# Kernel optimization log

Measured on AMD Instinct MI355X. Metric: run time of the kernel, lower is better.

## Reference

```python
import jax, jax.numpy as jnp
import numpy as np

N = 100000
E = 1600000
D_IN = 128
D_OUT = 128
NEG_SLOPE = 0.01  # PyTorch LeakyReLU default


def setup_inputs() -> dict:
    key = jax.random.key(0)
    ks = jax.random.split(key, 6)
    x = jax.random.normal(ks[0], (N, D_IN), dtype=jnp.float32)
    src = jax.random.randint(ks[1], (E,), 0, N, dtype=jnp.int32)
    dst = jax.random.randint(ks[2], (E,), 0, N, dtype=jnp.int32)
    e_attn = jax.random.uniform(ks[3], (E,), dtype=jnp.float32)
    # Xavier-normal-ish init for linear weights
    std = float(np.sqrt(2.0 / (D_IN + D_OUT)))
    W1 = jax.random.normal(ks[4], (D_OUT, D_IN), dtype=jnp.float32) * std
    W2 = jax.random.normal(ks[5], (D_OUT, D_IN), dtype=jnp.float32) * std
    b1 = jnp.zeros((D_OUT,), dtype=jnp.float32)
    b2 = jnp.zeros((D_OUT,), dtype=jnp.float32)
    return {"x": x, "src": src, "dst": dst, "e_attn": e_attn,
            "W1": W1, "b1": b1, "W2": W2, "b2": b2}


def leaky_relu(v):
    return jnp.where(v >= 0, v, NEG_SLOPE * v)


def reference(x, src, dst, e_attn, W1, b1, W2, b2):
    # Edge-weighted gather-scatter: h_n[d] = sum_{e: dst(e)=d} a_e * x[src(e)]
    msgs = x[src] * e_attn[:, None]                      # [E, D_IN]
    h_n = jax.ops.segment_sum(msgs, dst, num_segments=N)  # [N, D_IN]
    # Bi-interaction: LeakyReLU(W1(x + h_n)) + LeakyReLU(W2(x * h_n))
    add_part = leaky_relu(jnp.einsum('nd,od->no', x + h_n, W1) + b1)
    mul_part = leaky_relu(jnp.einsum('nd,od->no', x * h_n, W2) + b2)
    return add_part + mul_part  # dropout p=0.0 -> identity
```

## Files before the change

### kernel.cpp

```cpp
#include <hip/hip_runtime.h>

#define N_NODES 100000
#define E_EDGES 1600000
#define D 128
#define AP 132
#define ASTR 136

typedef short s16x8 __attribute__((ext_vector_type(8)));
typedef float f32x4 __attribute__((ext_vector_type(4)));

__device__ __forceinline__ unsigned short f2bf(float f) {
    union { float f; unsigned u; } v;
    v.f = f;
    unsigned r = v.u + 0x7FFFu + ((v.u >> 16) & 1u);
    return (unsigned short)(r >> 16);
}

__device__ __forceinline__ float bf2f(unsigned short u) {
    union { unsigned u; float f; } v;
    v.u = ((unsigned)u) << 16;
    return v.f;
}

__device__ __forceinline__ float lrelu(float v) {
    return v >= 0.0f ? v : 0.01f * v;
}

__global__ __launch_bounds__(256) void xconv_kernel(
    const float* __restrict__ x, unsigned short* __restrict__ xbf) {
    int idx = blockIdx.x * 256 + threadIdx.x;
    const float4* xp = (const float4*)(x) + (size_t)idx * 2;
    float4 a = xp[0], b = xp[1];
    ushort4 lo, hi;
    lo.x = f2bf(a.x); lo.y = f2bf(a.y); lo.z = f2bf(a.z); lo.w = f2bf(a.w);
    hi.x = f2bf(b.x); hi.y = f2bf(b.y); hi.z = f2bf(b.z); hi.w = f2bf(b.w);
    ushort4* dp = (ushort4*)(xbf) + (size_t)idx * 2;
    dp[0] = lo; dp[1] = hi;
}

__global__ __launch_bounds__(256) void hist_kernel(
    const int* __restrict__ dst, int* __restrict__ cnt,
    unsigned char* __restrict__ rank, int E, int stride) {
    int e = blockIdx.x * 256 + threadIdx.x;
    if (e < E) rank[e] = (unsigned char)atomicAdd(&cnt[(size_t)dst[e] * stride], 1);
}

__global__ __launch_bounds__(256) void scanA_kernel(
    const int* __restrict__ cnt, int* __restrict__ off,
    int* __restrict__ bsum, int n, int stride) {
    __shared__ int tmp[256];
    int gid = blockIdx.x * 256 + threadIdx.x;
    int v = (gid < n) ? cnt[(size_t)gid * stride] : 0;
    tmp[threadIdx.x] = v;
    __syncthreads();
    for (int ofs = 1; ofs < 256; ofs <<= 1) {
        int t = (threadIdx.x >= ofs) ? tmp[threadIdx.x - ofs] : 0;
        __syncthreads();
        tmp[threadIdx.x] += t;
        __syncthreads();
    }
    int incl = tmp[threadIdx.x];
    if (gid < n) off[gid] = incl - v;
    if (threadIdx.x == 255) bsum[blockIdx.x] = incl;
}

__global__ __launch_bounds__(512) void scanB_kernel(int* __restrict__ bsum, int nb) {
    __shared__ int tmp[512];
    int v = (threadIdx.x < nb) ? bsum[threadIdx.x] : 0;
    tmp[threadIdx.x] = v;
    __syncthreads();
    for (int ofs = 1; ofs < 512; ofs <<= 1) {
        int t = (threadIdx.x >= ofs) ? tmp[threadIdx.x - ofs] : 0;
        __syncthreads();
        tmp[threadIdx.x] += t;
        __syncthreads();
    }
    if (threadIdx.x < nb) bsum[threadIdx.x] = tmp[threadIdx.x] - v;
}

__global__ __launch_bounds__(256) void scanC_kernel(
    const int* __restrict__ bsumExcl, int* __restrict__ off, int n, int E) {
    int gid = blockIdx.x * 256 + threadIdx.x;
    if (gid < n) off[gid] += bsumExcl[gid >> 8];
    if (gid == 0) off[n] = E;
}

__global__ __launch_bounds__(256) void fill_kernel(
    const int* __restrict__ src, const int* __restrict__ dst,
    const float* __restrict__ ea, const int* __restrict__ off,
    const unsigned char* __restrict__ rank, int2* __restrict__ csr, int E) {
    int e = blockIdx.x * 256 + threadIdx.x;
    if (e >= E) return;
    int d = dst[e];
    int pos = off[d] + (int)rank[e];
    csr[pos] = make_int2(src[e], __float_as_int(ea[e]));
}

__global__ __launch_bounds__(256, 4) void fused_gemm_kernel(
    const unsigned short* __restrict__ xbf, const int2* __restrict__ csr,
    const int* __restrict__ off, const unsigned short* __restrict__ Wswz,
    const float* __restrict__ b1, const float* __restrict__ b2,
    float* __restrict__ out) {
    __shared__ unsigned short A[2][64 * ASTR];

    const int n0 = blockIdx.x * 64;
    const int t = threadIdx.x;
    const int lane = t & 63;
    const int wv = t >> 6;
    const int half = lane >> 5;
    const int li = lane & 31;

    s16x8 Bf[2][2][4];
    float bb1[2], bb2[2];
#pragma unroll
    for (int ci = 0; ci < 2; ++ci) {
        int ct = wv + ci * 4;
        bb1[ci] = b1[ct * 16 + (lane & 15)];
        bb2[ci] = b2[ct * 16 + (lane & 15)];
#pragma unroll
        for (int mat = 0; mat < 2; ++mat)
#pragma unroll
            for (int ks = 0; ks < 4; ++ks)
                Bf[ci][mat][ks] = *(const s16x8*)(
                    Wswz + ((size_t)(((mat * 4 + ks) * 8 + ct) * 64 + lane)) * 8);
    }

    for (int j = 0; j < 16; ++j) {
        int row = wv * 16 + j;
        int node = n0 + row;
        float4 hacc = make_float4(0.f, 0.f, 0.f, 0.f);
        if (node < N_NODES) {
            int beg = off[node];
            int end = off[node + 1];
            float4 acc1 = make_float4(0.f, 0.f, 0.f, 0.f);
            int i = beg + half;
            for (; i + 2 < end; i += 4) {
                int2 p0 = csr[i];
                int2 p1 = csr[i + 2];
                float a0 = __int_as_float(p0.y);
                float a1 = __int_as_float(p1.y);
                ushort4 v0 = ((const ushort4*)(xbf + (size_t)p0.x * D))[li];
                ushort4 v1 = ((const ushort4*)(xbf + (size_t)p1.x * D))[li];
                hacc.x += a0 * bf2f(v0.x); hacc.y += a0 * bf2f(v0.y);
                hacc.z += a0 * bf2f(v0.z); hacc.w += a0 * bf2f(v0.w);
                acc1.x += a1 * bf2f(v1.x); acc1.y += a1 * bf2f(v1.y);
                acc1.z += a1 * bf2f(v1.z); acc1.w += a1 * bf2f(v1.w);
            }
            if (i < end) {
                int2 p0 = csr[i];
                float a0 = __int_as_float(p0.y);
                ushort4 v0 = ((const ushort4*)(xbf + (size_t)p0.x * D))[li];
                hacc.x += a0 * bf2f(v0.x); hacc.y += a0 * bf2f(v0.y);
                hacc.z += a0 * bf2f(v0.z); hacc.w += a0 * bf2f(v0.w);
            }
            hacc.x += acc1.x; hacc.y += acc1.y;
            hacc.z += acc1.z; hacc.w += acc1.w;
        }
        float4 oth;
        oth.x = __shfl(hacc.x, lane ^ 32);
        oth.y = __shfl(hacc.y, lane ^ 32);
        oth.z = __shfl(hacc.z, lane ^ 32);
        oth.w = __shfl(hacc.w, lane ^ 32);
        hacc.x += oth.x; hacc.y += oth.y; hacc.z += oth.z; hacc.w += oth.w;

        if (half == 0) {
            ushort4 av, mv;
            if (node < N_NODES) {
                ushort4 xu = ((const ushort4*)(xbf + (size_t)node * D))[li];
                float4 xv = make_float4(bf2f(xu.x), bf2f(xu.y), bf2f(xu.z), bf2f(xu.w));
                av.x = f2bf(xv.x + hacc.x); av.y = f2bf(xv.y + hacc.y);
                av.z = f2bf(xv.z + hacc.z); av.w = f2bf(xv.w + hacc.w);
                mv.x = f2bf(xv.x * hacc.x); mv.y = f2bf(xv.y * hacc.y);
                mv.z = f2bf(xv.z * hacc.z); mv.w = f2bf(xv.w * hacc.w);
            } else {
                av = make_ushort4(0, 0, 0, 0);
                mv = make_ushort4(0, 0, 0, 0);
            }
            *(ushort4*)&A[0][row * ASTR + li * 4] = av;
            *(ushort4*)&A[1][row * ASTR + li * 4] = mv;
        }
    }

    __syncthreads();

    const int quad = lane >> 4;
    const int kq = quad * 8;

#pragma unroll
    for (int mt = 0; mt < 4; ++mt) {
        f32x4 acc[2][2];
#pragma unroll
        for (int ci = 0; ci < 2; ++ci)
#pragma unroll
            for (int p = 0; p < 2; ++p) acc[ci][p] = (f32x4){0.f, 0.f, 0.f, 0.f};

        const int arow = mt * 16 + (lane & 15);
#pragma unroll
        for (int ks = 0; ks < 4; ++ks) {
            s16x8 a0 = *(const s16x8*)&A[0][arow * ASTR + ks * 32 + kq];
            s16x8 a1 = *(const s16x8*)&A[1][arow * ASTR + ks * 32 + kq];
#pragma unroll
            for (int ci = 0; ci < 2; ++ci) {
                acc[ci][0] = __builtin_amdgcn_mfma_f32_16x16x32_bf16(
                    a0, Bf[ci][0][ks], acc[ci][0], 0, 0, 0);
                acc[ci][1] = __builtin_amdgcn_mfma_f32_16x16x32_bf16(
                    a1, Bf[ci][1][ks], acc[ci][1], 0, 0, 0);
            }
        }

#pragma unroll
        for (int ci = 0; ci < 2; ++ci) {
            int oc = (wv + ci * 4) * 16 + (lane & 15);
#pragma unroll
            for (int r = 0; r < 4; ++r) {
                int node = n0 + mt * 16 + quad * 4 + r;
                if (node < N_NODES) {
                    float v = lrelu(acc[ci][0][r] + bb1[ci])
                            + lrelu(acc[ci][1][r] + bb2[ci]);
                    out[(size_t)node * D + oc] = v;
                }
            }
        }
    }
}

__global__ __launch_bounds__(256) void gather_f32_kernel(
    const float* __restrict__ x, const int2* __restrict__ csr,
    const int* __restrict__ off, float* __restrict__ h) {
    int node = blockIdx.x * 4 + (threadIdx.x >> 6);
    int lane = threadIdx.x & 63;
    int beg = off[node];
    int end = off[node + 1];
    float2 acc0 = make_float2(0.f, 0.f);
    float2 acc1 = make_float2(0.f, 0.f);
    int e = beg;
    for (; e + 1 < end; e += 2) {
        int2 p0 = csr[e];
        int2 p1 = csr[e + 1];
        float a0 = __int_as_float(p0.y);
        float a1 = __int_as_float(p1.y);
        float2 v0 = ((const float2*)(x + (size_t)p0.x * D))[lane];
        float2 v1 = ((const float2*)(x + (size_t)p1.x * D))[lane];
        acc0.x += a0 * v0.x; acc0.y += a0 * v0.y;
        acc1.x += a1 * v1.x; acc1.y += a1 * v1.y;
    }
    if (e < end) {
        int2 p0 = csr[e];
        float a0 = __int_as_float(p0.y);
        float2 v0 = ((const float2*)(x + (size_t)p0.x * D))[lane];
        acc0.x += a0 * v0.x; acc0.y += a0 * v0.y;
    }
    acc0.x += acc1.x; acc0.y += acc1.y;
    ((float2*)(h + (size_t)node * D))[lane] = acc0;
}

__global__ __launch_bounds__(256) void scatter_kernel(
    const float* __restrict__ x, const int* __restrict__ src,
    const int* __restrict__ dst, const float* __restrict__ ea,
    float* __restrict__ h, int E) {
    int idx = blockIdx.x * 256 + threadIdx.x;
    int e = idx >> 5;
    int lane = idx & 31;
    if (e >= E) return;
    int s = src[e];
    int d = dst[e];
    float a = ea[e];
    float4 v = ((const float4*)(x + (size_t)s * D))[lane];
    float* hp = h + (size_t)d * D + lane * 4;
    atomicAdd(hp + 0, a * v.x);
    atomicAdd(hp + 1, a * v.y);
    atomicAdd(hp + 2, a * v.z);
    atomicAdd(hp + 3, a * v.w);
}

__global__ __launch_bounds__(256) void wconv_kernel(
    const float* __restrict__ W1, const float* __restrict__ W2,
    unsigned short* __restrict__ Wswz) {
    int tid = blockIdx.x * 256 + threadIdx.x;
    if (tid >= 2 * 4 * 8 * 64) return;
    int lane = tid & 63;
    int ct   = (tid >> 6) & 7;
    int ks   = (tid >> 9) & 3;
    int mat  = tid >> 11;
    const float* W = mat ? W2 : W1;
    int o  = ct * 16 + (lane & 15);
    int k0 = ks * 32 + (lane >> 4) * 8;
    const float* sp = W + (size_t)o * D + k0;
    unsigned short* dp = Wswz + (size_t)tid * 8;
    ushort4 lo, hi;
    lo.x = f2bf(sp[0]); lo.y = f2bf(sp[1]); lo.z = f2bf(sp[2]); lo.w = f2bf(sp[3]);
    hi.x = f2bf(sp[4]); hi.y = f2bf(sp[5]); hi.z = f2bf(sp[6]); hi.w = f2bf(sp[7]);
    *(ushort4*)(dp + 0) = lo;
    *(ushort4*)(dp + 4) = hi;
}

__global__ __launch_bounds__(256, 4) void mfma_gemm_kernel(
    const float* __restrict__ xf, const float* __restrict__ h,
    const unsigned short* __restrict__ Wswz,
    const float* __restrict__ b1, const float* __restrict__ b2,
    float* __restrict__ out) {
    __shared__ unsigned short A[2][64 * ASTR];

    const int n0 = blockIdx.x * 64;
    const int t = threadIdx.x;
    const int lane = t & 63;
    const int wv = t >> 6;

#pragma unroll
    for (int i = 0; i < 8; ++i) {
        int s = t + i * 256;
        int row = s >> 5;
        int c4 = s & 31;
        int srcrow = n0 + row;
        if (srcrow >= N_NODES) srcrow = N_NODES - 1;
        float4 xv = ((const float4*)(xf + (size_t)srcrow * D))[c4];
        float4 hv = ((const float4*)(h + (size_t)srcrow * D))[c4];
        ushort4 av, mv;
        av.x = f2bf(xv.x + hv.x); av.y = f2bf(xv.y + hv.y);
        av.z = f2bf(xv.z + hv.z); av.w = f2bf(xv.w + hv.w);
        mv.x = f2bf(xv.x * hv.x); mv.y = f2bf(xv.y * hv.y);
        mv.z = f2bf(xv.z * hv.z); mv.w = f2bf(xv.w * hv.w);
        *(ushort4*)&A[0][row * ASTR + c4 * 4] = av;
        *(ushort4*)&A[1][row * ASTR + c4 * 4] = mv;
    }

    s16x8 Bf[2][2][4];
    float bb1[2], bb2[2];
#pragma unroll
    for (int ci = 0; ci < 2; ++ci) {
        int ct = wv + ci * 4;
        bb1[ci] = b1[ct * 16 + (lane & 15)];
        bb2[ci] = b2[ct * 16 + (lane & 15)];
#pragma unroll
        for (int mat = 0; mat < 2; ++mat)
#pragma unroll
            for (int ks = 0; ks < 4; ++ks)
                Bf[ci][mat][ks] = *(const s16x8*)(
                    Wswz + ((size_t)(((mat * 4 + ks) * 8 + ct) * 64 + lane)) * 8);
    }

    __syncthreads();

    const int quad = lane >> 4;
    const int kq = quad * 8;

#pragma unroll
    for (int mt = 0; mt < 4; ++mt) {
        f32x4 acc[2][2];
#pragma unroll
        for (int ci = 0; ci < 2; ++ci)
#pragma unroll
            for (int p = 0; p < 2; ++p) acc[ci][p] = (f32x4){0.f, 0.f, 0.f, 0.f};

        const int arow = mt * 16 + (lane & 15);
#pragma unroll
        for (int ks = 0; ks < 4; ++ks) {
            s16x8 a0 = *(const s16x8*)&A[0][arow * ASTR + ks * 32 + kq];
            s16x8 a1 = *(const s16x8*)&A[1][arow * ASTR + ks * 32 + kq];
#pragma unroll
            for (int ci = 0; ci < 2; ++ci) {
                acc[ci][0] = __builtin_amdgcn_mfma_f32_16x16x32_bf16(
                    a0, Bf[ci][0][ks], acc[ci][0], 0, 0, 0);
                acc[ci][1] = __builtin_amdgcn_mfma_f32_16x16x32_bf16(
                    a1, Bf[ci][1][ks], acc[ci][1], 0, 0, 0);
            }
        }

#pragma unroll
        for (int ci = 0; ci < 2; ++ci) {
            int oc = (wv + ci * 4) * 16 + (lane & 15);
#pragma unroll
            for (int r = 0; r < 4; ++r) {
                int node = n0 + mt * 16 + quad * 4 + r;
                if (node < N_NODES) {
                    float v = lrelu(acc[ci][0][r] + bb1[ci])
                            + lrelu(acc[ci][1][r] + bb2[ci]);
                    out[(size_t)node * D + oc] = v;
                }
            }
        }
    }
}

__global__ __launch_bounds__(256) void gemm_kernel(
    const float* __restrict__ x, const float* __restrict__ h,
    const float* __restrict__ W1, const float* __restrict__ b1,
    const float* __restrict__ W2, const float* __restrict__ b2,
    float* __restrict__ out) {
    __shared__ float Aadd[32 * AP];
    __shared__ float Amul[32 * AP];
    const int n0 = blockIdx.x * 32;
    const int t = threadIdx.x;
#pragma unroll
    for (int i = 0; i < 4; ++i) {
        int fi = t + i * 256;
        int row = fi >> 5;
        int c4 = fi & 31;
        float4 xv = ((const float4*)(x + (size_t)(n0 + row) * D))[c4];
        float4 hv = ((const float4*)(h + (size_t)(n0 + row) * D))[c4];
        float4 av = make_float4(xv.x + hv.x, xv.y + hv.y, xv.z + hv.z, xv.w + hv.w);
        float4 mv = make_float4(xv.x * hv.x, xv.y * hv.y, xv.z * hv.z, xv.w * hv.w);
        *((float4*)&Aadd[row * AP + c4 * 4]) = av;
        *((float4*)&Amul[row * AP + c4 * 4]) = mv;
    }
    __syncthreads();
    const int m0 = (t >> 5) * 4;
    const int o0 = (t & 31) * 4;
    float acc1[4][4];
    float acc2[4][4];
#pragma unroll
    for (int i = 0; i < 4; ++i)
#pragma unroll
        for (int j = 0; j < 4; ++j) { acc1[i][j] = 0.0f; acc2[i][j] = 0.0f; }
#pragma unroll 4
    for (int d = 0; d < D; d += 4) {
        float4 a[4], m[4], w1[4], w2[4];
#pragma unroll
        for (int i = 0; i < 4; ++i) a[i] = *(const float4*)&Aadd[(m0 + i) * AP + d];
#pragma unroll
        for (int i = 0; i < 4; ++i) m[i] = *(const float4*)&Amul[(m0 + i) * AP + d];
#pragma unroll
        for (int j = 0; j < 4; ++j) w1[j] = *(const float4*)&W1[(size_t)(o0 + j) * D + d];
#pragma unroll
        for (int j = 0; j < 4; ++j) w2[j] = *(const float4*)&W2[(size_t)(o0 + j) * D + d];
#pragma unroll
        for (int i = 0; i < 4; ++i)
#pragma unroll
            for (int j = 0; j < 4; ++j) {
                acc1[i][j] += a[i].x * w1[j].x + a[i].y * w1[j].y
                            + a[i].z * w1[j].z + a[i].w * w1[j].w;
                acc2[i][j] += m[i].x * w2[j].x + m[i].y * w2[j].y
                            + m[i].z * w2[j].z + m[i].w * w2[j].w;
            }
    }
#pragma unroll
    for (int i = 0; i < 4; ++i) {
        float4 r;
        float v1, v2;
        v1 = lrelu(acc1[i][0] + b1[o0 + 0]); v2 = lrelu(acc2[i][0] + b2[o0 + 0]); r.x = v1 + v2;
        v1 = lrelu(acc1[i][1] + b1[o0 + 1]); v2 = lrelu(acc2[i][1] + b2[o0 + 1]); r.y = v1 + v2;
        v1 = lrelu(acc1[i][2] + b1[o0 + 2]); v2 = lrelu(acc2[i][2] + b2[o0 + 2]); r.z = v1 + v2;
        v1 = lrelu(acc1[i][3] + b1[o0 + 3]); v2 = lrelu(acc2[i][3] + b2[o0 + 3]); r.w = v1 + v2;
        ((float4*)(out + (size_t)(n0 + m0 + i) * D))[t & 31] = r;
    }
}

extern "C" void kernel_launch(void* const* d_in, const int* in_sizes, int n_in,
                              void* d_out, int out_size, void* d_ws, size_t ws_size,
                              hipStream_t stream) {
    const float* x   = (const float*)d_in[0];
    const int*   src = (const int*)d_in[1];
    const int*   dst = (const int*)d_in[2];
    const float* ea  = (const float*)d_in[3];
    const float* W1  = (const float*)d_in[4];
    const float* b1  = (const float*)d_in[5];
    const float* W2  = (const float*)d_in[6];
    const float* b2  = (const float*)d_in[7];
    float* out = (float*)d_out;

    auto align256 = [](size_t v) { return (v + 255) & ~(size_t)255; };

    const size_t SZ_WSWZ = 2 * 4 * 8 * 64 * 8 * sizeof(unsigned short);
    const size_t SZ_OFF  = (size_t)(N_NODES + 1) * sizeof(int);
    const size_t SZ_BSUM = 512 * sizeof(int);
    const size_t SZ_RANK = (size_t)E_EDGES;
    const size_t SZ_CSR  = (size_t)E_EDGES * sizeof(int2);
    const size_t SZ_XBF  = (size_t)N_NODES * D * sizeof(unsigned short);

    struct Lay { size_t o_wswz, o_cnt, o_off, o_bsum, o_rank, o_csr, o_xbf,
                 need_fused, need_t1, sz_cnt; };
    auto mk = [&](int stride) {
        Lay L;
        L.sz_cnt = (size_t)N_NODES * stride * sizeof(int);
        L.o_wswz = 0;
        L.o_cnt  = L.o_wswz + align256(SZ_WSWZ);
        L.o_off  = L.o_cnt + align256(L.sz_cnt);
        L.o_bsum = L.o_off + align256(SZ_OFF);
        L.o_rank = L.o_bsum + align256(SZ_BSUM);
        L.o_csr  = L.o_rank + align256(SZ_RANK);
        L.o_xbf  = L.o_csr + align256(SZ_CSR);
        L.need_t1 = L.o_xbf;
        L.need_fused = L.o_xbf + align256(SZ_XBF);
        return L;
    };

    Lay L16 = mk(16), L1 = mk(1);
    int stride;
    Lay L;
    bool fused_ok, t1_ok;
    if (ws_size >= L16.need_fused)      { stride = 16; L = L16; fused_ok = true;  t1_ok = true; }
    else if (ws_size >= L1.need_fused)  { stride = 1;  L = L1;  fused_ok = true;  t1_ok = true; }
    else if (ws_size >= L1.need_t1)     { stride = 1;  L = L1;  fused_ok = false; t1_ok = true; }
    else                                { stride = 1;  L = L1;  fused_ok = false; t1_ok = false; }

    const int NB_E = (E_EDGES + 255) / 256;
    const int NB_N = (N_NODES + 255) / 256;

    char* ws = (char*)d_ws;
    unsigned short* Wswz = (unsigned short*)(ws + L.o_wswz);
    int*   cnt  = (int*)(ws + L.o_cnt);
    int*   off  = (int*)(ws + L.o_off);
    int*   bsum = (int*)(ws + L.o_bsum);
    unsigned char* rank = (unsigned char*)(ws + L.o_rank);
    int2*  csr  = (int2*)(ws + L.o_csr);
    unsigned short* xbf = (unsigned short*)(ws + L.o_xbf);

    if (t1_ok) {
        hipMemsetAsync(cnt, 0, L.sz_cnt, stream);
        if (fused_ok)
            xconv_kernel<<<(N_NODES * D / 8 + 255) / 256, 256, 0, stream>>>(x, xbf);
        hist_kernel<<<NB_E, 256, 0, stream>>>(dst, cnt, rank, E_EDGES, stride);
        scanA_kernel<<<NB_N, 256, 0, stream>>>(cnt, off, bsum, N_NODES, stride);
        scanB_kernel<<<1, 512, 0, stream>>>(bsum, NB_N);
        scanC_kernel<<<NB_N, 256, 0, stream>>>(bsum, off, N_NODES, E_EDGES);
        fill_kernel<<<NB_E, 256, 0, stream>>>(src, dst, ea, off, rank, csr, E_EDGES);
        wconv_kernel<<<16, 256, 0, stream>>>(W1, W2, Wswz);

        int blocks = (N_NODES + 63) / 64;
        if (fused_ok) {
            fused_gemm_kernel<<<blocks, 256, 0, stream>>>(xbf, csr, off, Wswz,
                                                          b1, b2, out);
        } else {
            float* h = out;
            gather_f32_kernel<<<N_NODES / 4, 256, 0, stream>>>(x, csr, off, h);
            mfma_gemm_kernel<<<blocks, 256, 0, stream>>>(x, h, Wswz, b1, b2, out);
        }
    } else {
        float* h = out;
        hipMemsetAsync(h, 0, (size_t)N_NODES * D * sizeof(float), stream);
        int total = E_EDGES * 32;
        scatter_kernel<<<(total + 255) / 256, 256, 0, stream>>>(x, src, dst, ea,
                                                                h, E_EDGES);
        gemm_kernel<<<N_NODES / 32, 256, 0, stream>>>(x, h, W1, b1, W2, b2, out);
    }
}
```

Measured before the change: 377.1 us.

## Split gather from GEMM, widen gather loads, merge prep and fill launches

The fused gather-plus-GEMM kernel is split in two. A standalone gather kernel uses one wave per node, 16-byte bf16 row loads and four edge streams in parallel, then writes the aggregated h as bf16 (or fp32 in a lower workspace tier). The GEMM kernel then loads x and h tiles cooperatively before its MFMA loop. The histogram, x conversion and weight swizzle kernels are merged into one launch, and the scan fix-up is folded into the CSR fill kernel, to cut launch count. The aim is more memory-level parallelism in the irregular gather; the cost is an extra h round-trip through global memory and an extra bf16 rounding of h.

```diff
diff --git a/kernel.cpp b/kernel.cpp
--- a/kernel.cpp
+++ b/kernel.cpp
@@ -7,6 +7,7 @@
 #define ASTR 136
 
 typedef short s16x8 __attribute__((ext_vector_type(8)));
+typedef unsigned short u16x8 __attribute__((ext_vector_type(8)));
 typedef float f32x4 __attribute__((ext_vector_type(4)));
 
 __device__ __forceinline__ unsigned short f2bf(float f) {
@@ -26,27 +27,46 @@
     return v >= 0.0f ? v : 0.01f * v;
 }
 
-__global__ __launch_bounds__(256) void xconv_kernel(
-    const float* __restrict__ x, unsigned short* __restrict__ xbf) {
-    int idx = blockIdx.x * 256 + threadIdx.x;
-    const float4* xp = (const float4*)(x) + (size_t)idx * 2;
-    float4 a = xp[0], b = xp[1];
-    ushort4 lo, hi;
-    lo.x = f2bf(a.x); lo.y = f2bf(a.y); lo.z = f2bf(a.z); lo.w = f2bf(a.w);
-    hi.x = f2bf(b.x); hi.y = f2bf(b.y); hi.z = f2bf(b.z); hi.w = f2bf(b.w);
-    ushort4* dp = (ushort4*)(xbf) + (size_t)idx * 2;
-    dp[0] = lo; dp[1] = hi;
-}
-
-__global__ __launch_bounds__(256) void hist_kernel(
+__global__ __launch_bounds__(256) void prep_kernel(
     const int* __restrict__ dst, int* __restrict__ cnt,
-    unsigned char* __restrict__ rank, int E, int stride) {
-    int e = blockIdx.x * 256 + threadIdx.x;
-    if (e < E) rank[e] = (unsigned char)atomicAdd(&cnt[(size_t)dst[e] * stride], 1);
+    unsigned char* __restrict__ rank, int stride,
+    const float* __restrict__ x, unsigned short* __restrict__ xbf, int do_xconv,
+    const float* __restrict__ W1, const float* __restrict__ W2,
+    unsigned short* __restrict__ Wswz) {
+    int b = blockIdx.x;
+    int t = threadIdx.x;
+    if (b < 6250) {
+        int e = b * 256 + t;
+        rank[e] = (unsigned char)atomicAdd(&cnt[(size_t)dst[e] * stride], 1);
+    } else if (b < 12500) {
+        if (!do_xconv) return;
+        int idx = (b - 6250) * 256 + t;
+        const float4* xp = (const float4*)(x) + (size_t)idx * 2;
+        float4 a = xp[0], bb = xp[1];
+        u16x8 o;
+        o[0] = f2bf(a.x);  o[1] = f2bf(a.y);  o[2] = f2bf(a.z);  o[3] = f2bf(a.w);
+        o[4] = f2bf(bb.x); o[5] = f2bf(bb.y); o[6] = f2bf(bb.z); o[7] = f2bf(bb.w);
+        ((u16x8*)(xbf))[idx] = o;
+    } else {
+        int tid = (b - 12500) * 256 + t;
+        if (tid >= 2 * 4 * 8 * 64) return;
+        int lane = tid & 63;
+        int ct   = (tid >> 6) & 7;
+        int ks   = (tid >> 9) & 3;
+        int mat  = tid >> 11;
+        const float* W = mat ? W2 : W1;
+        int o  = ct * 16 + (lane & 15);
+        int k0 = ks * 32 + (lane >> 4) * 8;
+        const float* sp = W + (size_t)o * D + k0;
+        u16x8 w;
+#pragma unroll
+        for (int j = 0; j < 8; ++j) w[j] = f2bf(sp[j]);
+        ((u16x8*)(Wswz))[tid] = w;
+    }
 }
 
 __global__ __launch_bounds__(256) void scanA_kernel(
-    const int* __restrict__ cnt, int* __restrict__ off,
+    const int* __restrict__ cnt, int* __restrict__ excl,
     int* __restrict__ bsum, int n, int stride) {
     __shared__ int tmp[256];
     int gid = blockIdx.x * 256 + threadIdx.x;
@@ -60,7 +80,7 @@
         __syncthreads();
     }
     int incl = tmp[threadIdx.x];
-    if (gid < n) off[gid] = incl - v;
+    if (gid < n) excl[gid] = incl - v;
     if (threadIdx.x == 255) bsum[blockIdx.x] = incl;
 }
 
@@ -78,27 +98,82 @@
     if (threadIdx.x < nb) bsum[threadIdx.x] = tmp[threadIdx.x] - v;
 }
 
-__global__ __launch_bounds__(256) void scanC_kernel(
-    const int* __restrict__ bsumExcl, int* __restrict__ off, int n, int E) {
+__global__ __launch_bounds__(256) void fillC_kernel(
+    const int* __restrict__ src, const int* __restrict__ dst,
+    const float* __restrict__ ea, const int* __restrict__ excl,
+    const int* __restrict__ bsum, const unsigned char* __restrict__ rank,
+    int2* __restrict__ csr, int* __restrict__ off) {
     int gid = blockIdx.x * 256 + threadIdx.x;
-    if (gid < n) off[gid] += bsumExcl[gid >> 8];
-    if (gid == 0) off[n] = E;
-}
-
-__global__ __launch_bounds__(256) void fill_kernel(
-    const int* __restrict__ src, const int* __restrict__ dst,
-    const float* __restrict__ ea, const int* __restrict__ off,
-    const unsigned char* __restrict__ rank, int2* __restrict__ csr, int E) {
-    int e = blockIdx.x * 256 + threadIdx.x;
-    if (e >= E) return;
-    int d = dst[e];
-    int pos = off[d] + (int)rank[e];
-    csr[pos] = make_int2(src[e], __float_as_int(ea[e]));
-}
-
-__global__ __launch_bounds__(256, 4) void fused_gemm_kernel(
+    int d = dst[gid];
+    int pos = excl[d] + bsum[d >> 8] + (int)rank[gid];
+    csr[pos] = make_int2(src[gid], __float_as_int(ea[gid]));
+    if (gid < N_NODES) off[gid] = excl[gid] + bsum[gid >> 8];
+    else if (gid == N_NODES) off[N_NODES] = E_EDGES;
+}
+
+template <bool HBF16>
+__global__ __launch_bounds__(256) void gather16_kernel(
     const unsigned short* __restrict__ xbf, const int2* __restrict__ csr,
-    const int* __restrict__ off, const unsigned short* __restrict__ Wswz,
+    const int* __restrict__ off, unsigned short* __restrict__ hbf,
+    float* __restrict__ hf) {
+    int node = blockIdx.x * 4 + (threadIdx.x >> 6);
+    int lane = threadIdx.x & 63;
+    int q = lane >> 4;
+    int li = lane & 15;
+    int beg = off[node];
+    int end = off[node + 1];
+
+    float a0[8], a1[8];
+#pragma unroll
+    for (int d = 0; d < 8; ++d) { a0[d] = 0.f; a1[d] = 0.f; }
+
+    int i = beg + q;
+    for (; i + 4 < end; i += 8) {
+        int2 p0 = csr[i];
+        int2 p1 = csr[i + 4];
+        float w0 = __int_as_float(p0.y);
+        float w1 = __int_as_float(p1.y);
+        u16x8 v0 = ((const u16x8*)(xbf + (size_t)p0.x * D))[li];
+        u16x8 v1 = ((const u16x8*)(xbf + (size_t)p1.x * D))[li];
+#pragma unroll
+        for (int d = 0; d < 8; ++d) {
+            a0[d] += w0 * bf2f(v0[d]);
+            a1[d] += w1 * bf2f(v1[d]);
+        }
+    }
+    if (i < end) {
+        int2 p0 = csr[i];
+        float w0 = __int_as_float(p0.y);
+        u16x8 v0 = ((const u16x8*)(xbf + (size_t)p0.x * D))[li];
+#pragma unroll
+        for (int d = 0; d < 8; ++d) a0[d] += w0 * bf2f(v0[d]);
+    }
+#pragma unroll
+    for (int d = 0; d < 8; ++d) a0[d] += a1[d];
+#pragma unroll
+    for (int d = 0; d < 8; ++d) a0[d] += __shfl_xor(a0[d], 16);
+#pragma unroll
+    for (int d = 0; d < 8; ++d) a0[d] += __shfl_xor(a0[d], 32);
+
+    if (q == 0) {
+        if (HBF16) {
+            u16x8 o;
+#pragma unroll
+            for (int d = 0; d < 8; ++d) o[d] = f2bf(a0[d]);
+            ((u16x8*)(hbf + (size_t)node * D))[li] = o;
+        } else {
+            float4 lo = make_float4(a0[0], a0[1], a0[2], a0[3]);
+            float4 hi = make_float4(a0[4], a0[5], a0[6], a0[7]);
+            ((float4*)(hf + (size_t)node * D))[li * 2 + 0] = lo;
+            ((float4*)(hf + (size_t)node * D))[li * 2 + 1] = hi;
+        }
+    }
+}
+
+template <bool HBF16>
+__global__ __launch_bounds__(256, 4) void mfma_gemm_bfh_kernel(
+    const unsigned short* __restrict__ xbf, const unsigned short* __restrict__ hbf,
+    const float* __restrict__ hf, const unsigned short* __restrict__ Wswz,
     const float* __restrict__ b1, const float* __restrict__ b2,
     float* __restrict__ out) {
     __shared__ unsigned short A[2][64 * ASTR];
@@ -107,8 +182,36 @@
     const int t = threadIdx.x;
     const int lane = t & 63;
     const int wv = t >> 6;
-    const int half = lane >> 5;
-    const int li = lane & 31;
+
+#pragma unroll
+    for (int i = 0; i < 4; ++i) {
+        int s = t + i * 256;
+        int row = s >> 4;
+        int c8 = s & 15;
+        int srcrow = n0 + row;
+        if (srcrow >= N_NODES) srcrow = N_NODES - 1;
+        u16x8 xu = ((const u16x8*)(xbf + (size_t)srcrow * D))[c8];
+        float hd[8];
+        if (HBF16) {
+            u16x8 hu = ((const u16x8*)(hbf + (size_t)srcrow * D))[c8];
+#pragma unroll
+            for (int j = 0; j < 8; ++j) hd[j] = bf2f(hu[j]);
+        } else {
+            float4 h0 = ((const float4*)(hf + (size_t)srcrow * D))[c8 * 2 + 0];
+            float4 h1 = ((const float4*)(hf + (size_t)srcrow * D))[c8 * 2 + 1];
+            hd[0] = h0.x; hd[1] = h0.y; hd[2] = h0.z; hd[3] = h0.w;
+            hd[4] = h1.x; hd[5] = h1.y; hd[6] = h1.z; hd[7] = h1.w;
+        }
+        u16x8 av, mv;
+#pragma unroll
+        for (int j = 0; j < 8; ++j) {
+            float xv = bf2f(xu[j]);
+            av[j] = f2bf(xv + hd[j]);
+            mv[j] = f2bf(xv * hd[j]);
+        }
+        *(u16x8*)&A[0][row * ASTR + c8 * 8] = av;
+        *(u16x8*)&A[1][row * ASTR + c8 * 8] = mv;
+    }
 
     s16x8 Bf[2][2][4];
     float bb1[2], bb2[2];
@@ -125,62 +228,6 @@
                     Wswz + ((size_t)(((mat * 4 + ks) * 8 + ct) * 64 + lane)) * 8);
     }
 
-    for (int j = 0; j < 16; ++j) {
-        int row = wv * 16 + j;
-        int node = n0 + row;
-        float4 hacc = make_float4(0.f, 0.f, 0.f, 0.f);
-        if (node < N_NODES) {
-            int beg = off[node];
-            int end = off[node + 1];
-            float4 acc1 = make_float4(0.f, 0.f, 0.f, 0.f);
-            int i = beg + half;
-            for (; i + 2 < end; i += 4) {
-                int2 p0 = csr[i];
-                int2 p1 = csr[i + 2];
-                float a0 = __int_as_float(p0.y);
-                float a1 = __int_as_float(p1.y);
-                ushort4 v0 = ((const ushort4*)(xbf + (size_t)p0.x * D))[li];
-                ushort4 v1 = ((const ushort4*)(xbf + (size_t)p1.x * D))[li];
-                hacc.x += a0 * bf2f(v0.x); hacc.y += a0 * bf2f(v0.y);
-                hacc.z += a0 * bf2f(v0.z); hacc.w += a0 * bf2f(v0.w);
-                acc1.x += a1 * bf2f(v1.x); acc1.y += a1 * bf2f(v1.y);
-                acc1.z += a1 * bf2f(v1.z); acc1.w += a1 * bf2f(v1.w);
-            }
-            if (i < end) {
-                int2 p0 = csr[i];
-                float a0 = __int_as_float(p0.y);
-                ushort4 v0 = ((const ushort4*)(xbf + (size_t)p0.x * D))[li];
-                hacc.x += a0 * bf2f(v0.x); hacc.y += a0 * bf2f(v0.y);
-                hacc.z += a0 * bf2f(v0.z); hacc.w += a0 * bf2f(v0.w);
-            }
-            hacc.x += acc1.x; hacc.y += acc1.y;
-            hacc.z += acc1.z; hacc.w += acc1.w;
-        }
-        float4 oth;
-        oth.x = __shfl(hacc.x, lane ^ 32);
-        oth.y = __shfl(hacc.y, lane ^ 32);
-        oth.z = __shfl(hacc.z, lane ^ 32);
-        oth.w = __shfl(hacc.w, lane ^ 32);
-        hacc.x += oth.x; hacc.y += oth.y; hacc.z += oth.z; hacc.w += oth.w;
-
-        if (half == 0) {
-            ushort4 av, mv;
-            if (node < N_NODES) {
-                ushort4 xu = ((const ushort4*)(xbf + (size_t)node * D))[li];
-                float4 xv = make_float4(bf2f(xu.x), bf2f(xu.y), bf2f(xu.z), bf2f(xu.w));
-                av.x = f2bf(xv.x + hacc.x); av.y = f2bf(xv.y + hacc.y);
-                av.z = f2bf(xv.z + hacc.z); av.w = f2bf(xv.w + hacc.w);
-                mv.x = f2bf(xv.x * hacc.x); mv.y = f2bf(xv.y * hacc.y);
-                mv.z = f2bf(xv.z * hacc.z); mv.w = f2bf(xv.w * hacc.w);
-            } else {
-                av = make_ushort4(0, 0, 0, 0);
-                mv = make_ushort4(0, 0, 0, 0);
-            }
-            *(ushort4*)&A[0][row * ASTR + li * 4] = av;
-            *(ushort4*)&A[1][row * ASTR + li * 4] = mv;
-        }
-    }
-
     __syncthreads();
 
     const int quad = lane >> 4;
@@ -197,14 +244,14 @@
         const int arow = mt * 16 + (lane & 15);
 #pragma unroll
         for (int ks = 0; ks < 4; ++ks) {
-            s16x8 a0 = *(const s16x8*)&A[0][arow * ASTR + ks * 32 + kq];
-            s16x8 a1 = *(const s16x8*)&A[1][arow * ASTR + ks * 32 + kq];
+            s16x8 aa0 = *(const s16x8*)&A[0][arow * ASTR + ks * 32 + kq];
+            s16x8 aa1 = *(const s16x8*)&A[1][arow * ASTR + ks * 32 + kq];
 #pragma unroll
             for (int ci = 0; ci < 2; ++ci) {
                 acc[ci][0] = __builtin_amdgcn_mfma_f32_16x16x32_bf16(
-                    a0, Bf[ci][0][ks], acc[ci][0], 0, 0, 0);
+                    aa0, Bf[ci][0][ks], acc[ci][0], 0, 0, 0);
                 acc[ci][1] = __builtin_amdgcn_mfma_f32_16x16x32_bf16(
-                    a1, Bf[ci][1][ks], acc[ci][1], 0, 0, 0);
+                    aa1, Bf[ci][1][ks], acc[ci][1], 0, 0, 0);
             }
         }
 
@@ -254,6 +301,86 @@
     ((float2*)(h + (size_t)node * D))[lane] = acc0;
 }
 
+__global__ __launch_bounds__(256, 4) void mfma_gemm_t1_kernel(
+    const float* __restrict__ xf, const float* __restrict__ h,
+    const unsigned short* __restrict__ Wswz,
+    const float* __restrict__ b1, const float* __restrict__ b2,
+    float* __restrict__ out) {
+    __shared__ unsigned short A[2][64 * ASTR];
+    const int n0 = blockIdx.x * 64;
+    const int t = threadIdx.x;
+    const int lane = t & 63;
+    const int wv = t >> 6;
+#pragma unroll
+    for (int i = 0; i < 8; ++i) {
+        int s = t + i * 256;
+        int row = s >> 5;
+        int c4 = s & 31;
+        int srcrow = n0 + row;
+        if (srcrow >= N_NODES) srcrow = N_NODES - 1;
+        float4 xv = ((const float4*)(xf + (size_t)srcrow * D))[c4];
+        float4 hv = ((const float4*)(h + (size_t)srcrow * D))[c4];
+        ushort4 av, mv;
+        av.x = f2bf(xv.x + hv.x); av.y = f2bf(xv.y + hv.y);
+        av.z = f2bf(xv.z + hv.z); av.w = f2bf(xv.w + hv.w);
+        mv.x = f2bf(xv.x * hv.x); mv.y = f2bf(xv.y * hv.y);
+        mv.z = f2bf(xv.z * hv.z); mv.w = f2bf(xv.w * hv.w);
+        *(ushort4*)&A[0][row * ASTR + c4 * 4] = av;
+        *(ushort4*)&A[1][row * ASTR + c4 * 4] = mv;
+    }
+    s16x8 Bf[2][2][4];
+    float bb1[2], bb2[2];
+#pragma unroll
+    for (int ci = 0; ci < 2; ++ci) {
+        int ct = wv + ci * 4;
+        bb1[ci] = b1[ct * 16 + (lane & 15)];
+        bb2[ci] = b2[ct * 16 + (lane & 15)];
+#pragma unroll
+        for (int mat = 0; mat < 2; ++mat)
+#pragma unroll
+            for (int ks = 0; ks < 4; ++ks)
+                Bf[ci][mat][ks] = *(const s16x8*)(
+                    Wswz + ((size_t)(((mat * 4 + ks) * 8 + ct) * 64 + lane)) * 8);
+    }
+    __syncthreads();
+    const int quad = lane >> 4;
+    const int kq = quad * 8;
+#pragma unroll
+    for (int mt = 0; mt < 4; ++mt) {
+        f32x4 acc[2][2];
+#pragma unroll
+        for (int ci = 0; ci < 2; ++ci)
+#pragma unroll
+            for (int p = 0; p < 2; ++p) acc[ci][p] = (f32x4){0.f, 0.f, 0.f, 0.f};
+        const int arow = mt * 16 + (lane & 15);
+#pragma unroll
+        for (int ks = 0; ks < 4; ++ks) {
+            s16x8 aa0 = *(const s16x8*)&A[0][arow * ASTR + ks * 32 + kq];
+            s16x8 aa1 = *(const s16x8*)&A[1][arow * ASTR + ks * 32 + kq];
+#pragma unroll
+            for (int ci = 0; ci < 2; ++ci) {
+                acc[ci][0] = __builtin_amdgcn_mfma_f32_16x16x32_bf16(
+                    aa0, Bf[ci][0][ks], acc[ci][0], 0, 0, 0);
+                acc[ci][1] = __builtin_amdgcn_mfma_f32_16x16x32_bf16(
+                    aa1, Bf[ci][1][ks], acc[ci][1], 0, 0, 0);
+            }
+        }
+#pragma unroll
+        for (int ci = 0; ci < 2; ++ci) {
+            int oc = (wv + ci * 4) * 16 + (lane & 15);
+#pragma unroll
+            for (int r = 0; r < 4; ++r) {
+                int node = n0 + mt * 16 + quad * 4 + r;
+                if (node < N_NODES) {
+                    float v = lrelu(acc[ci][0][r] + bb1[ci])
+                            + lrelu(acc[ci][1][r] + bb2[ci]);
+                    out[(size_t)node * D + oc] = v;
+                }
+            }
+        }
+    }
+}
+
 __global__ __launch_bounds__(256) void scatter_kernel(
     const float* __restrict__ x, const int* __restrict__ src,
     const int* __restrict__ dst, const float* __restrict__ ea,
@@ -273,115 +400,6 @@
     atomicAdd(hp + 3, a * v.w);
 }
 
-__global__ __launch_bounds__(256) void wconv_kernel(
-    const float* __restrict__ W1, const float* __restrict__ W2,
-    unsigned short* __restrict__ Wswz) {
-    int tid = blockIdx.x * 256 + threadIdx.x;
-    if (tid >= 2 * 4 * 8 * 64) return;
-    int lane = tid & 63;
-    int ct   = (tid >> 6) & 7;
-    int ks   = (tid >> 9) & 3;
-    int mat  = tid >> 11;
-    const float* W = mat ? W2 : W1;
-    int o  = ct * 16 + (lane & 15);
-    int k0 = ks * 32 + (lane >> 4) * 8;
-    const float* sp = W + (size_t)o * D + k0;
-    unsigned short* dp = Wswz + (size_t)tid * 8;
-    ushort4 lo, hi;
-    lo.x = f2bf(sp[0]); lo.y = f2bf(sp[1]); lo.z = f2bf(sp[2]); lo.w = f2bf(sp[3]);
-    hi.x = f2bf(sp[4]); hi.y = f2bf(sp[5]); hi.z = f2bf(sp[6]); hi.w = f2bf(sp[7]);
-    *(ushort4*)(dp + 0) = lo;
-    *(ushort4*)(dp + 4) = hi;
-}
-
-__global__ __launch_bounds__(256, 4) void mfma_gemm_kernel(
-    const float* __restrict__ xf, const float* __restrict__ h,
-    const unsigned short* __restrict__ Wswz,
-    const float* __restrict__ b1, const float* __restrict__ b2,
-    float* __restrict__ out) {
-    __shared__ unsigned short A[2][64 * ASTR];
-
-    const int n0 = blockIdx.x * 64;
-    const int t = threadIdx.x;
-    const int lane = t & 63;
-    const int wv = t >> 6;
-
-#pragma unroll
-    for (int i = 0; i < 8; ++i) {
-        int s = t + i * 256;
-        int row = s >> 5;
-        int c4 = s & 31;
-        int srcrow = n0 + row;
-        if (srcrow >= N_NODES) srcrow = N_NODES - 1;
-        float4 xv = ((const float4*)(xf + (size_t)srcrow * D))[c4];
-        float4 hv = ((const float4*)(h + (size_t)srcrow * D))[c4];
-        ushort4 av, mv;
-        av.x = f2bf(xv.x + hv.x); av.y = f2bf(xv.y + hv.y);
-        av.z = f2bf(xv.z + hv.z); av.w = f2bf(xv.w + hv.w);
-        mv.x = f2bf(xv.x * hv.x); mv.y = f2bf(xv.y * hv.y);
-        mv.z = f2bf(xv.z * hv.z); mv.w = f2bf(xv.w * hv.w);
-        *(ushort4*)&A[0][row * ASTR + c4 * 4] = av;
-        *(ushort4*)&A[1][row * ASTR + c4 * 4] = mv;
-    }
-
-    s16x8 Bf[2][2][4];
-    float bb1[2], bb2[2];
-#pragma unroll
-    for (int ci = 0; ci < 2; ++ci) {
-        int ct = wv + ci * 4;
-        bb1[ci] = b1[ct * 16 + (lane & 15)];
-        bb2[ci] = b2[ct * 16 + (lane & 15)];
-#pragma unroll
-        for (int mat = 0; mat < 2; ++mat)
-#pragma unroll
-            for (int ks = 0; ks < 4; ++ks)
-                Bf[ci][mat][ks] = *(const s16x8*)(
-                    Wswz + ((size_t)(((mat * 4 + ks) * 8 + ct) * 64 + lane)) * 8);
-    }
-
-    __syncthreads();
-
-    const int quad = lane >> 4;
-    const int kq = quad * 8;
-
-#pragma unroll
-    for (int mt = 0; mt < 4; ++mt) {
-        f32x4 acc[2][2];
-#pragma unroll
-        for (int ci = 0; ci < 2; ++ci)
-#pragma unroll
-            for (int p = 0; p < 2; ++p) acc[ci][p] = (f32x4){0.f, 0.f, 0.f, 0.f};
-
-        const int arow = mt * 16 + (lane & 15);
-#pragma unroll
-        for (int ks = 0; ks < 4; ++ks) {
-            s16x8 a0 = *(const s16x8*)&A[0][arow * ASTR + ks * 32 + kq];
-            s16x8 a1 = *(const s16x8*)&A[1][arow * ASTR + ks * 32 + kq];
-#pragma unroll
-            for (int ci = 0; ci < 2; ++ci) {
-                acc[ci][0] = __builtin_amdgcn_mfma_f32_16x16x32_bf16(
-                    a0, Bf[ci][0][ks], acc[ci][0], 0, 0, 0);
-                acc[ci][1] = __builtin_amdgcn_mfma_f32_16x16x32_bf16(
-                    a1, Bf[ci][1][ks], acc[ci][1], 0, 0, 0);
-            }
-        }
-
-#pragma unroll
-        for (int ci = 0; ci < 2; ++ci) {
-            int oc = (wv + ci * 4) * 16 + (lane & 15);
-#pragma unroll
-            for (int r = 0; r < 4; ++r) {
-                int node = n0 + mt * 16 + quad * 4 + r;
-                if (node < N_NODES) {
-                    float v = lrelu(acc[ci][0][r] + bb1[ci])
-                            + lrelu(acc[ci][1][r] + bb2[ci]);
-                    out[(size_t)node * D + oc] = v;
-                }
-            }
-        }
-    }
-}
-
 __global__ __launch_bounds__(256) void gemm_kernel(
     const float* __restrict__ x, const float* __restrict__ h,
     const float* __restrict__ W1, const float* __restrict__ b1,
@@ -462,68 +480,83 @@
 
     const size_t SZ_WSWZ = 2 * 4 * 8 * 64 * 8 * sizeof(unsigned short);
     const size_t SZ_OFF  = (size_t)(N_NODES + 1) * sizeof(int);
+    const size_t SZ_EXCL = (size_t)N_NODES * sizeof(int);
     const size_t SZ_BSUM = 512 * sizeof(int);
     const size_t SZ_RANK = (size_t)E_EDGES;
     const size_t SZ_CSR  = (size_t)E_EDGES * sizeof(int2);
     const size_t SZ_XBF  = (size_t)N_NODES * D * sizeof(unsigned short);
-
-    struct Lay { size_t o_wswz, o_cnt, o_off, o_bsum, o_rank, o_csr, o_xbf,
-                 need_fused, need_t1, sz_cnt; };
+    const size_t SZ_HBF  = SZ_XBF;
+
+    struct Lay { size_t o_wswz, o_cnt, o_off, o_excl, o_bsum, o_rank, o_csr,
+                 o_xbf, o_hbf, need_t1, need_t2, need_t3, sz_cnt; };
     auto mk = [&](int stride) {
         Lay L;
         L.sz_cnt = (size_t)N_NODES * stride * sizeof(int);
         L.o_wswz = 0;
         L.o_cnt  = L.o_wswz + align256(SZ_WSWZ);
         L.o_off  = L.o_cnt + align256(L.sz_cnt);
-        L.o_bsum = L.o_off + align256(SZ_OFF);
+        L.o_excl = L.o_off + align256(SZ_OFF);
+        L.o_bsum = L.o_excl + align256(SZ_EXCL);
         L.o_rank = L.o_bsum + align256(SZ_BSUM);
         L.o_csr  = L.o_rank + align256(SZ_RANK);
         L.o_xbf  = L.o_csr + align256(SZ_CSR);
+        L.o_hbf  = L.o_xbf + align256(SZ_XBF);
         L.need_t1 = L.o_xbf;
-        L.need_fused = L.o_xbf + align256(SZ_XBF);
+        L.need_t2 = L.o_hbf;
+        L.need_t3 = L.o_hbf + align256(SZ_HBF);
         return L;
     };
 
     Lay L16 = mk(16), L1 = mk(1);
+    int tier;
+    Lay L;
     int stride;
-    Lay L;
-    bool fused_ok, t1_ok;
-    if (ws_size >= L16.need_fused)      { stride = 16; L = L16; fused_ok = true;  t1_ok = true; }
-    else if (ws_size >= L1.need_fused)  { stride = 1;  L = L1;  fused_ok = true;  t1_ok = true; }
-    else if (ws_size >= L1.need_t1)     { stride = 1;  L = L1;  fused_ok = false; t1_ok = true; }
-    else                                { stride = 1;  L = L1;  fused_ok = false; t1_ok = false; }
-
-    const int NB_E = (E_EDGES + 255) / 256;
-    const int NB_N = (N_NODES + 255) / 256;
+    if (ws_size >= L16.need_t3)      { tier = 3; L = L16; stride = 16; }
+    else if (ws_size >= L16.need_t2) { tier = 2; L = L16; stride = 16; }
+    else if (ws_size >= L1.need_t2)  { tier = 2; L = L1;  stride = 1; }
+    else if (ws_size >= L1.need_t1)  { tier = 1; L = L1;  stride = 1; }
+    else                             { tier = 0; L = L1;  stride = 1; }
 
     char* ws = (char*)d_ws;
     unsigned short* Wswz = (unsigned short*)(ws + L.o_wswz);
     int*   cnt  = (int*)(ws + L.o_cnt);
     int*   off  = (int*)(ws + L.o_off);
+    int*   excl = (int*)(ws + L.o_excl);
     int*   bsum = (int*)(ws + L.o_bsum);
     unsigned char* rank = (unsigned char*)(ws + L.o_rank);
     int2*  csr  = (int2*)(ws + L.o_csr);
     unsigned short* xbf = (unsigned short*)(ws + L.o_xbf);
-
-    if (t1_ok) {
+    unsigned short* hbf = (unsigned short*)(ws + L.o_hbf);
+
+    const int NB_E = 6250;
+    const int NB_N = (N_NODES + 255) / 256;
+    const int GEMM_BLOCKS = (N_NODES + 63) / 64;
+
+    if (tier >= 1) {
         hipMemsetAsync(cnt, 0, L.sz_cnt, stream);
-        if (fused_ok)
-            xconv_kernel<<<(N_NODES * D / 8 + 255) / 256, 256, 0, stream>>>(x, xbf);
-        hist_kernel<<<NB_E, 256, 0, stream>>>(dst, cnt, rank, E_EDGES, stride);
-        scanA_kernel<<<NB_N, 256, 0, stream>>>(cnt, off, bsum, N_NODES, stride);
+        prep_kernel<<<12516, 256, 0, stream>>>(dst, cnt, rank, stride,
+                                               x, xbf, tier >= 2 ? 1 : 0,
+                                               W1, W2, Wswz);
+        scanA_kernel<<<NB_N, 256, 0, stream>>>(cnt, excl, bsum, N_NODES, stride);
         scanB_kernel<<<1, 512, 0, stream>>>(bsum, NB_N);
-        scanC_kernel<<<NB_N, 256, 0, stream>>>(bsum, off, N_NODES, E_EDGES);
-        fill_kernel<<<NB_E, 256, 0, stream>>>(src, dst, ea, off, rank, csr, E_EDGES);
-        wconv_kernel<<<16, 256, 0, stream>>>(W1, W2, Wswz);
-
-        int blocks = (N_NODES + 63) / 64;
-        if (fused_ok) {
-            fused_gemm_kernel<<<blocks, 256, 0, stream>>>(xbf, csr, off, Wswz,
-                                                          b1, b2, out);
+        fillC_kernel<<<NB_E, 256, 0, stream>>>(src, dst, ea, excl, bsum, rank,
+                                               csr, off);
+        if (tier == 3) {
+            gather16_kernel<true><<<N_NODES / 4, 256, 0, stream>>>(xbf, csr, off,
+                                                                   hbf, nullptr);
+            mfma_gemm_bfh_kernel<true><<<GEMM_BLOCKS, 256, 0, stream>>>(
+                xbf, hbf, nullptr, Wswz, b1, b2, out);
+        } else if (tier == 2) {
+            float* h = out;
+            gather16_kernel<false><<<N_NODES / 4, 256, 0, stream>>>(xbf, csr, off,
+                                                                    nullptr, h);
+            mfma_gemm_bfh_kernel<false><<<GEMM_BLOCKS, 256, 0, stream>>>(
+                xbf, nullptr, h, Wswz, b1, b2, out);
         } else {
             float* h = out;
             gather_f32_kernel<<<N_NODES / 4, 256, 0, stream>>>(x, csr, off, h);
-            mfma_gemm_kernel<<<blocks, 256, 0, stream>>>(x, h, Wswz, b1, b2, out);
+            mfma_gemm_t1_kernel<<<GEMM_BLOCKS, 256, 0, stream>>>(x, h, Wswz,
+                                                                 b1, b2, out);
         }
     } else {
         float* h = out;
```

New measurement: 305.8 us. 18.9% less time.
